# Performance work log

Measured on AMD Instinct MI355X. Metric: run time of the kernel, lower is better.

Reference implementation:

```python
import jax, jax.numpy as jnp
import numpy as np


def setup_inputs() -> dict:
    key = jax.random.key(0)
    k0, k1, k2, k3 = jax.random.split(key, 4)
    B, T, M, E, H = 4, 2048, 1024, 8, 4096
    x = jax.random.normal(k0, (B, T, M), dtype=jnp.float32)
    wg = jax.random.normal(k1, (M, E), dtype=jnp.float32) * 0.02
    w1 = jax.random.normal(k2, (E, M, H), dtype=jnp.float32) * 0.02
    w2 = jax.random.normal(k3, (E, H, M), dtype=jnp.float32) * 0.02
    return {"x": x, "wg": wg, "w1": w1, "w2": w2}


def reference(x, wg, w1, w2):
    """GShard MoE layer: top-1 gate + dense one-hot dispatch/combine + expert FFN."""
    M = x.shape[-1]
    xs = x.reshape(-1, M)                      # [s, m]
    s = xs.shape[0]
    E = wg.shape[1]
    capacity = s // E                          # capacity_factor = 1.0

    # ---- top-1 gate (deepspeed/gshard top1gating) ----
    logits = xs @ wg                           # [s, e]
    gates = jax.nn.softmax(logits, axis=-1)
    idx = jnp.argmax(gates, axis=1)            # [s]
    mask1 = jax.nn.one_hot(idx, E, dtype=gates.dtype)  # [s, e]
    me = gates.mean(axis=0)
    ce = mask1.mean(axis=0)
    l_aux = jnp.sum(me * ce) * E
    # position of each token within its expert's buffer
    locations = jnp.cumsum(mask1, axis=0) - 1.0          # [s, e]
    mask1 = mask1 * (locations < capacity).astype(gates.dtype)  # drop overflow
    gates1 = gates * mask1                                 # [s, e]
    loc_s = jnp.sum(locations * mask1, axis=1).astype(jnp.int32)  # [s]
    loc_sc = jax.nn.one_hot(loc_s, capacity, dtype=gates.dtype)   # [s, c]
    combine = gates1[:, :, None] * loc_sc[:, None, :]       # [s, e, c]
    dispatch = (combine > 0).astype(x.dtype)                # [s, e, c]

    # ---- dense one-hot dispatch (the kernel-headroom hotspot) ----
    dispatched = jnp.einsum('sec,sm->ecm', dispatch, xs)    # [e, c, m]

    # ---- per-expert 2-layer FFN ----
    h = jax.nn.relu(jnp.einsum('ecm,emh->ech', dispatched, w1))
    expert_out = jnp.einsum('ech,ehm->ecm', h, w2)          # [e, c, m]

    # ---- dense one-hot combine ----
    out = jnp.einsum('sec,ecm->sm', combine, expert_out).reshape(x.shape)
    return out, l_aux
```

## Files before the change

kernel.cpp:

```cpp
#include <hip/hip_runtime.h>
#include <hip/hip_bf16.h>

#define S_TOK 8192
#define MDIM  1024
#define EXP   8
#define HDIM  4096
#define CAP   1024

typedef __attribute__((ext_vector_type(8))) short short8;
typedef __attribute__((ext_vector_type(4))) float floatx4;

__device__ __forceinline__ unsigned short f2b(float f) {
    union { float f; unsigned int i; } v; v.f = f;
    unsigned int r = v.i + 0x7fffu + ((v.i >> 16) & 1u);
    return (unsigned short)(r >> 16);
}

__global__ __launch_bounds__(256) void gate_kernel(
    const float* __restrict__ x, const float* __restrict__ wg,
    float* __restrict__ gates8, int* __restrict__ token_expert)
{
    const int wave = threadIdx.x >> 6, lane = threadIdx.x & 63;
    const int s = blockIdx.x * 4 + wave;

    const float* xr = x + (size_t)s * MDIM + lane * 16;
    float xv[16];
#pragma unroll
    for (int q = 0; q < 4; ++q) *(float4*)(xv + q * 4) = *(const float4*)(xr + q * 4);

    float acc[EXP];
#pragma unroll
    for (int e = 0; e < EXP; ++e) acc[e] = 0.f;
    const int m0 = lane * 16;
#pragma unroll
    for (int j = 0; j < 16; ++j) {
        const float xm = xv[j];
        const float* wr = wg + (size_t)(m0 + j) * EXP;
        float4 w0 = *(const float4*)(wr);
        float4 w1v = *(const float4*)(wr + 4);
        acc[0] += xm * w0.x; acc[1] += xm * w0.y; acc[2] += xm * w0.z; acc[3] += xm * w0.w;
        acc[4] += xm * w1v.x; acc[5] += xm * w1v.y; acc[6] += xm * w1v.z; acc[7] += xm * w1v.w;
    }
#pragma unroll
    for (int e = 0; e < EXP; ++e) {
#pragma unroll
        for (int off = 32; off > 0; off >>= 1)
            acc[e] += __shfl_down(acc[e], off);
    }
    if (lane == 0) {
        float mx = acc[0]; int idx = 0;
#pragma unroll
        for (int e = 1; e < EXP; ++e) if (acc[e] > mx) { mx = acc[e]; idx = e; }
        float g[EXP]; float sum = 0.f;
#pragma unroll
        for (int e = 0; e < EXP; ++e) { g[e] = expf(acc[e] - mx); sum += g[e]; }
        float inv = 1.f / sum;
#pragma unroll
        for (int e = 0; e < EXP; ++e) gates8[(size_t)s * EXP + e] = g[e] * inv;
        token_expert[s] = idx;
    }
}

__global__ __launch_bounds__(256) void scan_kernel(
    const float* __restrict__ gates8, const int* __restrict__ token_expert,
    int* __restrict__ slot_token, float* __restrict__ slot_gate,
    float* __restrict__ laux_out)
{
    __shared__ int   cnt[256][EXP];
    __shared__ float fsum[256][EXP];
    __shared__ int   tot[EXP];
    const int t = threadIdx.x;

    for (int i = t; i < EXP * CAP; i += 256) slot_token[i] = -1;

    int local[EXP];
#pragma unroll
    for (int e = 0; e < EXP; ++e) local[e] = 0;
    const int s0 = t * 32;
    for (int j = 0; j < 32; ++j) local[token_expert[s0 + j]]++;
#pragma unroll
    for (int e = 0; e < EXP; ++e) cnt[t][e] = local[e];
    __syncthreads();

    if (t < EXP) {
        int run = 0;
        for (int i = 0; i < 256; ++i) { int v = cnt[i][t]; cnt[i][t] = run; run += v; }
        tot[t] = run;
    }
    __syncthreads();

    int off[EXP];
#pragma unroll
    for (int e = 0; e < EXP; ++e) off[e] = cnt[t][e];
    for (int j = 0; j < 32; ++j) {
        int s = s0 + j;
        int e = token_expert[s];
        int loc = off[e]++;
        if (loc < CAP) {
            int slot = e * CAP + loc;
            slot_token[slot] = s;
            slot_gate[slot]  = gates8[(size_t)s * EXP + e];
        }
    }

    float ms[EXP];
#pragma unroll
    for (int e = 0; e < EXP; ++e) ms[e] = 0.f;
    for (int j = 0; j < 32; ++j) {
        const float* g = gates8 + (size_t)(s0 + j) * EXP;
#pragma unroll
        for (int e = 0; e < EXP; ++e) ms[e] += g[e];
    }
#pragma unroll
    for (int e = 0; e < EXP; ++e) fsum[t][e] = ms[e];
    __syncthreads();
    for (int st = 128; st > 0; st >>= 1) {
        if (t < st) {
#pragma unroll
            for (int e = 0; e < EXP; ++e) fsum[t][e] += fsum[t + st][e];
        }
        __syncthreads();
    }
    if (t == 0) {
        float l = 0.f;
#pragma unroll
        for (int e = 0; e < EXP; ++e)
            l += (fsum[0][e] / (float)S_TOK) * ((float)tot[e] / (float)S_TOK);
        laux_out[0] = l * (float)EXP;
    }
}

__global__ __launch_bounds__(256) void dispatch_cvt(
    const float* __restrict__ x, const int* __restrict__ slot_token,
    unsigned short* __restrict__ xd)
{
    const int slot = blockIdx.x, t = threadIdx.x;
    const int tok = slot_token[slot];
    unsigned short v[4];
    if (tok >= 0) {
        float4 f = *(const float4*)(x + (size_t)tok * MDIM + t * 4);
        v[0] = f2b(f.x); v[1] = f2b(f.y); v[2] = f2b(f.z); v[3] = f2b(f.w);
    } else {
        v[0] = v[1] = v[2] = v[3] = 0;
    }
    *(int2*)(xd + (size_t)slot * MDIM + t * 4) = *(const int2*)v;
}

__global__ __launch_bounds__(256) void transpose_cvt(
    const float* __restrict__ src, unsigned short* __restrict__ dst, int R, int C)
{
    __shared__ unsigned short Ls[64 * 72];
    const size_t eo = (size_t)blockIdx.z * R * C;
    src += eo; dst += eo;
    const int C0 = blockIdx.x * 64, R0 = blockIdx.y * 64;
    const int t = threadIdx.x;
    {
        const int r = t >> 2, c0 = (t & 3) * 16;
        const float* p = src + (size_t)(R0 + r) * C + C0 + c0;
        float f[16];
#pragma unroll
        for (int q = 0; q < 4; ++q) *(float4*)(f + q * 4) = ((const float4*)p)[q];
#pragma unroll
        for (int j = 0; j < 16; ++j) Ls[(c0 + j) * 72 + r] = f2b(f[j]);
    }
    __syncthreads();
    {
        const int c = t >> 2, m0 = (t & 3) * 16;
        int4 v0 = *(const int4*)&Ls[c * 72 + m0];
        int4 v1 = *(const int4*)&Ls[c * 72 + m0 + 8];
        int4* q = (int4*)(dst + (size_t)(C0 + c) * R + R0 + m0);
        q[0] = v0; q[1] = v1;
    }
}

template<int KSTEPS, int N, bool SCATTER>
__global__ __launch_bounds__(256) void ffn_gemm_fast(
    const unsigned short* __restrict__ Ab, const unsigned short* __restrict__ BT,
    void* __restrict__ Outv,
    const int* __restrict__ slot_token, const float* __restrict__ slot_gate)
{
    constexpr int K = KSTEPS * 32;
    const int e  = blockIdx.z;
    const int ib = blockIdx.y * 128;
    const int nb = blockIdx.x * 128;
    const int t  = threadIdx.x;

    __shared__ unsigned short As[128 * 40];
    __shared__ unsigned short Bs[128 * 40];

    const int row = t >> 1, half = t & 1;
    const unsigned short* Ap = Ab + ((size_t)e * CAP + ib + row) * K + half * 16;
    const unsigned short* Bp = BT + ((size_t)e * N   + nb + row) * K + half * 16;

    const int lane = t & 63, wave = t >> 6;
    const int quad = lane >> 4, l15 = lane & 15;
    const int wr = wave >> 1, wc = wave & 1;

    floatx4 acc[4][4];
#pragma unroll
    for (int r = 0; r < 4; ++r)
#pragma unroll
        for (int c = 0; c < 4; ++c)
            acc[r][c] = (floatx4){0.f, 0.f, 0.f, 0.f};

    for (int kb = 0; kb < KSTEPS; ++kb) {
        const int k0 = kb * 32;
        int4 a0 = ((const int4*)(Ap + k0))[0];
        int4 a1 = ((const int4*)(Ap + k0))[1];
        int4 b0 = ((const int4*)(Bp + k0))[0];
        int4 b1 = ((const int4*)(Bp + k0))[1];

        *(int4*)&As[row * 40 + half * 16]     = a0;
        *(int4*)&As[row * 40 + half * 16 + 8] = a1;
        *(int4*)&Bs[row * 40 + half * 16]     = b0;
        *(int4*)&Bs[row * 40 + half * 16 + 8] = b1;
        __syncthreads();

        short8 af[4], bfr[4];
#pragma unroll
        for (int r = 0; r < 4; ++r)
            af[r] = *(const short8*)&As[(wr * 64 + r * 16 + l15) * 40 + quad * 8];
#pragma unroll
        for (int c = 0; c < 4; ++c)
            bfr[c] = *(const short8*)&Bs[(wc * 64 + c * 16 + l15) * 40 + quad * 8];
#pragma unroll
        for (int r = 0; r < 4; ++r)
#pragma unroll
            for (int c = 0; c < 4; ++c)
                acc[r][c] = __builtin_amdgcn_mfma_f32_16x16x32_bf16(af[r], bfr[c], acc[r][c], 0, 0, 0);
        __syncthreads();
    }

#pragma unroll
    for (int r = 0; r < 4; ++r) {
#pragma unroll
        for (int reg = 0; reg < 4; ++reg) {
            const int gi = ib + wr * 64 + r * 16 + quad * 4 + reg;
            if (SCATTER) {
                const int slot = e * CAP + gi;
                const int tok = slot_token[slot];
                if (tok >= 0) {
                    const float gsc = slot_gate[slot];
                    float* Out = (float*)Outv;
#pragma unroll
                    for (int c = 0; c < 4; ++c) {
                        const int gn = nb + wc * 64 + c * 16 + l15;
                        Out[(size_t)tok * N + gn] = gsc * acc[r][c][reg];
                    }
                }
            } else {
                unsigned short* Out = (unsigned short*)Outv;
#pragma unroll
                for (int c = 0; c < 4; ++c) {
                    const int gn = nb + wc * 64 + c * 16 + l15;
                    Out[((size_t)e * CAP + gi) * N + gn] = f2b(fmaxf(acc[r][c][reg], 0.f));
                }
            }
        }
    }
}

template<int KSTEPS, int N, bool GATHER, bool SCATTER>
__global__ __launch_bounds__(256) void ffn_gemm_slow(
    const void* __restrict__ Agv, const float* __restrict__ Bg,
    void* __restrict__ Outv,
    const int* __restrict__ slot_token, const float* __restrict__ slot_gate)
{
    constexpr int K = KSTEPS * 32;
    const int e  = blockIdx.z;
    const int ib = blockIdx.y * 128;
    const int nb = blockIdx.x * 128;
    const int t  = threadIdx.x;

    __shared__ unsigned short As[128 * 40];
    __shared__ unsigned short Bs[32 * 136];

    const float* B = Bg + (size_t)e * K * N;
    const int arow  = t >> 1;
    const int ahalf = t & 1;
    const float* ArowF = nullptr;
    const unsigned short* ArowH = nullptr;
    bool avalid = true;
    if (GATHER) {
        int tok = slot_token[e * CAP + ib + arow];
        avalid = (tok >= 0);
        ArowF = (const float*)Agv + (size_t)(avalid ? tok : 0) * K;
    } else {
        ArowH = (const unsigned short*)Agv + ((size_t)e * CAP + ib + arow) * K;
    }
    const int bk  = t >> 3;
    const int bn0 = (t & 7) * 16;
    const float* Bptr = B + (size_t)bk * N + nb + bn0;

    const int lane = t & 63, wave = t >> 6;
    const int quad = lane >> 4, l15 = lane & 15;
    const int wr = wave >> 1, wc = wave & 1;

    floatx4 acc[4][4];
#pragma unroll
    for (int r = 0; r < 4; ++r)
#pragma unroll
        for (int c = 0; c < 4; ++c)
            acc[r][c] = (floatx4){0.f, 0.f, 0.f, 0.f};

    for (int kb = 0; kb < KSTEPS; ++kb) {
        const int k0 = kb * 32;
        unsigned short av[16];
        if (GATHER) {
            if (avalid) {
                const float4* p = (const float4*)(ArowF + k0 + ahalf * 16);
                float4 f0 = p[0], f1 = p[1], f2 = p[2], f3 = p[3];
                const float fa[16] = {f0.x,f0.y,f0.z,f0.w, f1.x,f1.y,f1.z,f1.w,
                                      f2.x,f2.y,f2.z,f2.w, f3.x,f3.y,f3.z,f3.w};
#pragma unroll
                for (int j = 0; j < 16; ++j) av[j] = f2b(fa[j]);
            } else {
#pragma unroll
                for (int j = 0; j < 16; ++j) av[j] = 0;
            }
        } else {
            const int4* p = (const int4*)(ArowH + k0 + ahalf * 16);
            *(int4*)(av)     = p[0];
            *(int4*)(av + 8) = p[1];
        }
        unsigned short bv[16];
        {
            const float4* q = (const float4*)(Bptr + (size_t)k0 * N);
            float4 f0 = q[0], f1 = q[1], f2 = q[2], f3 = q[3];
            const float fb[16] = {f0.x,f0.y,f0.z,f0.w, f1.x,f1.y,f1.z,f1.w,
                                  f2.x,f2.y,f2.z,f2.w, f3.x,f3.y,f3.z,f3.w};
#pragma unroll
            for (int j = 0; j < 16; ++j) bv[j] = f2b(fb[j]);
        }

        *(int4*)&As[arow * 40 + ahalf * 16]     = *(int4*)(av);
        *(int4*)&As[arow * 40 + ahalf * 16 + 8] = *(int4*)(av + 8);
        *(int4*)&Bs[bk * 136 + bn0]             = *(int4*)(bv);
        *(int4*)&Bs[bk * 136 + bn0 + 8]         = *(int4*)(bv + 8);
        __syncthreads();

        short8 af[4];
#pragma unroll
        for (int r = 0; r < 4; ++r)
            af[r] = *(const short8*)&As[(wr * 64 + r * 16 + l15) * 40 + quad * 8];
        short8 bfr[4];
#pragma unroll
        for (int c = 0; c < 4; ++c) {
#pragma unroll
            for (int j = 0; j < 8; ++j)
                bfr[c][j] = (short)Bs[(quad * 8 + j) * 136 + wc * 64 + c * 16 + l15];
        }
#pragma unroll
        for (int r = 0; r < 4; ++r)
#pragma unroll
            for (int c = 0; c < 4; ++c)
                acc[r][c] = __builtin_amdgcn_mfma_f32_16x16x32_bf16(af[r], bfr[c], acc[r][c], 0, 0, 0);
        __syncthreads();
    }

#pragma unroll
    for (int r = 0; r < 4; ++r) {
#pragma unroll
        for (int reg = 0; reg < 4; ++reg) {
            const int gi = ib + wr * 64 + r * 16 + quad * 4 + reg;
            if (SCATTER) {
                const int slot = e * CAP + gi;
                const int tok = slot_token[slot];
                if (tok >= 0) {
                    const float gsc = slot_gate[slot];
                    float* Out = (float*)Outv;
#pragma unroll
                    for (int c = 0; c < 4; ++c) {
                        const int gn = nb + wc * 64 + c * 16 + l15;
                        Out[(size_t)tok * N + gn] = gsc * acc[r][c][reg];
                    }
                }
            } else {
                unsigned short* Out = (unsigned short*)Outv;
#pragma unroll
                for (int c = 0; c < 4; ++c) {
                    const int gn = nb + wc * 64 + c * 16 + l15;
                    Out[((size_t)e * CAP + gi) * N + gn] = f2b(fmaxf(acc[r][c][reg], 0.f));
                }
            }
        }
    }
}

extern "C" void kernel_launch(void* const* d_in, const int* in_sizes, int n_in,
                              void* d_out, int out_size, void* d_ws, size_t ws_size,
                              hipStream_t stream)
{
    const float* x  = (const float*)d_in[0];
    const float* wg = (const float*)d_in[1];
    const float* w1 = (const float*)d_in[2];
    const float* w2 = (const float*)d_in[3];
    float* out = (float*)d_out;

    char* ws = (char*)d_ws;
    float* gates8       = (float*)(ws);
    int*   token_expert = (int*)(ws + 262144);
    int*   slot_token   = (int*)(ws + 294912);
    float* slot_gate    = (float*)(ws + 327680);

    hipMemsetAsync(d_out, 0, (size_t)out_size * 4, stream);
    gate_kernel<<<dim3(S_TOK / 4), dim3(256), 0, stream>>>(x, wg, gates8, token_expert);
    scan_kernel<<<dim3(1), dim3(256), 0, stream>>>(gates8, token_expert, slot_token, slot_gate,
                                                   out + (size_t)S_TOK * MDIM);

    const size_t FAST_NEED = 151355392ull;
    if (ws_size >= FAST_NEED) {
        unsigned short* xd = (unsigned short*)(ws + 360448);
        unsigned short* h  = (unsigned short*)(ws + 17137664);
        unsigned short* W  = (unsigned short*)(ws + 84246528);

        dispatch_cvt<<<dim3(EXP * CAP), dim3(256), 0, stream>>>(x, slot_token, xd);
        transpose_cvt<<<dim3(HDIM / 64, MDIM / 64, EXP), dim3(256), 0, stream>>>(w1, W, MDIM, HDIM);
        ffn_gemm_fast<32, HDIM, false><<<dim3(HDIM / 128, CAP / 128, EXP), dim3(256), 0, stream>>>(
            xd, W, h, slot_token, slot_gate);
        transpose_cvt<<<dim3(MDIM / 64, HDIM / 64, EXP), dim3(256), 0, stream>>>(w2, W, HDIM, MDIM);
        ffn_gemm_fast<128, MDIM, true><<<dim3(MDIM / 128, CAP / 128, EXP), dim3(256), 0, stream>>>(
            h, W, out, slot_token, slot_gate);
    } else {
        unsigned short* h = (unsigned short*)(ws + 360448);
        ffn_gemm_slow<32, HDIM, true, false><<<dim3(HDIM / 128, CAP / 128, EXP), dim3(256), 0, stream>>>(
            x, w1, h, slot_token, slot_gate);
        ffn_gemm_slow<128, MDIM, false, true><<<dim3(MDIM / 128, CAP / 128, EXP), dim3(256), 0, stream>>>(
            h, w2, out, slot_token, slot_gate);
    }
}
```

Before: 632.3 us.

## Double-buffer FFN GEMM tiles using direct global-to-LDS loads

Replaces the register-staged global loads and LDS stores in the expert FFN GEMM with direct global_load_lds transfers into two alternating LDS buffers. The next K-slice is fetched while MFMAs run on the current one, which removes one barrier per iteration and the VGPR round trip. The padded stride-40 layout becomes an unpadded stride-32 layout, which risks LDS bank conflicts on the fragment reads and doubles LDS use. Correctness depends on the hardware's wave-ordered placement for global_load_lds and on the barrier also waiting for the outstanding vmcnt.

```diff
diff --git a/kernel.cpp b/kernel.cpp
--- a/kernel.cpp
+++ b/kernel.cpp
@@ -14,6 +14,13 @@
     union { float f; unsigned int i; } v; v.f = f;
     unsigned int r = v.i + 0x7fffu + ((v.i >> 16) & 1u);
     return (unsigned short)(r >> 16);
+}
+
+__device__ __forceinline__ void gl2lds16(const unsigned short* g, unsigned short* l) {
+    __builtin_amdgcn_global_load_lds(
+        (const __attribute__((address_space(1))) unsigned int*)g,
+        (__attribute__((address_space(3))) unsigned int*)l,
+        16, 0, 0);
 }
 
 __global__ __launch_bounds__(256) void gate_kernel(
@@ -185,17 +192,22 @@
     const int nb = blockIdx.x * 128;
     const int t  = threadIdx.x;
 
-    __shared__ unsigned short As[128 * 40];
-    __shared__ unsigned short Bs[128 * 40];
-
-    const int row = t >> 1, half = t & 1;
-    const unsigned short* Ap = Ab + ((size_t)e * CAP + ib + row) * K + half * 16;
-    const unsigned short* Bp = BT + ((size_t)e * N   + nb + row) * K + half * 16;
+    __shared__ unsigned short As[2][128 * 32];
+    __shared__ unsigned short Bs[2][128 * 32];
 
     const int lane = t & 63, wave = t >> 6;
     const int quad = lane >> 4, l15 = lane & 15;
     const int wr = wave >> 1, wc = wave & 1;
 
+    const int c0    = wave * 2;
+    const int srow  = lane >> 2;
+    const int kpart = (lane & 3) * 8;
+
+    const unsigned short* Ag = Ab + (size_t)(e * CAP + ib) * K + kpart;
+    const unsigned short* Bg = BT + ((size_t)e * N + nb) * K + kpart;
+    const size_t row0 = (size_t)(c0 * 16 + srow) * K;
+    const size_t row1 = (size_t)(c0 * 16 + 16 + srow) * K;
+
     floatx4 acc[4][4];
 #pragma unroll
     for (int r = 0; r < 4; ++r)
@@ -203,32 +215,36 @@
         for (int c = 0; c < 4; ++c)
             acc[r][c] = (floatx4){0.f, 0.f, 0.f, 0.f};
 
+    auto stage = [&](int buf, int kb) {
+        const int k0 = kb * 32;
+        gl2lds16(Ag + row0 + k0, &As[buf][(c0    ) * 512]);
+        gl2lds16(Ag + row1 + k0, &As[buf][(c0 + 1) * 512]);
+        gl2lds16(Bg + row0 + k0, &Bs[buf][(c0    ) * 512]);
+        gl2lds16(Bg + row1 + k0, &Bs[buf][(c0 + 1) * 512]);
+    };
+
+    int cur = 0;
+    stage(0, 0);
+    __syncthreads();
+
     for (int kb = 0; kb < KSTEPS; ++kb) {
-        const int k0 = kb * 32;
-        int4 a0 = ((const int4*)(Ap + k0))[0];
-        int4 a1 = ((const int4*)(Ap + k0))[1];
-        int4 b0 = ((const int4*)(Bp + k0))[0];
-        int4 b1 = ((const int4*)(Bp + k0))[1];
-
-        *(int4*)&As[row * 40 + half * 16]     = a0;
-        *(int4*)&As[row * 40 + half * 16 + 8] = a1;
-        *(int4*)&Bs[row * 40 + half * 16]     = b0;
-        *(int4*)&Bs[row * 40 + half * 16 + 8] = b1;
-        __syncthreads();
+        if (kb + 1 < KSTEPS) stage(cur ^ 1, kb + 1);
 
         short8 af[4], bfr[4];
 #pragma unroll
         for (int r = 0; r < 4; ++r)
-            af[r] = *(const short8*)&As[(wr * 64 + r * 16 + l15) * 40 + quad * 8];
+            af[r] = *(const short8*)&As[cur][(wr * 64 + r * 16 + l15) * 32 + quad * 8];
 #pragma unroll
         for (int c = 0; c < 4; ++c)
-            bfr[c] = *(const short8*)&Bs[(wc * 64 + c * 16 + l15) * 40 + quad * 8];
+            bfr[c] = *(const short8*)&Bs[cur][(wc * 64 + c * 16 + l15) * 32 + quad * 8];
 #pragma unroll
         for (int r = 0; r < 4; ++r)
 #pragma unroll
             for (int c = 0; c < 4; ++c)
                 acc[r][c] = __builtin_amdgcn_mfma_f32_16x16x32_bf16(af[r], bfr[c], acc[r][c], 0, 0, 0);
+
         __syncthreads();
+        cur ^= 1;
     }
 
 #pragma unroll
```

After: 622.3 us. Within noise of the previous version (-1.6%).
